# Kernel tuning notes

Hardware: AMD Instinct MI355X
Metric: run time of the kernel (lower is better)

Reference implementation:

```python
import jax, jax.numpy as jnp
import numpy as np

VOCAB, D, H1, H2, T = 32000, 256, 256, 256, 12
PAD, START, STOP = 0, 10, 11
B, S, NS = 32, 512, 16


def setup_inputs() -> dict:
    key = jax.random.key(0)
    ks = jax.random.split(key, 16)
    def rn(k, shape, scale=0.1):
        return (jax.random.normal(k, shape) * scale).astype(jnp.float32)
    inputs = jax.random.randint(ks[0], (B, S), 0, VOCAB)
    sent_embs = jax.random.normal(ks[1], (B, NS, 2 * H1), dtype=jnp.float32)
    embed = rn(ks[2], (VOCAB, D)).at[0].set(0.0)  # padding_idx=0
    # BiLSTM 1: input D, hidden H1; gate order i,f,g,o; dim 0 = [fwd, bwd]
    lstm1_wih = rn(ks[3], (2, 4 * H1, D))
    lstm1_whh = rn(ks[4], (2, 4 * H1, H1))
    lstm1_b = rn(ks[5], (2, 4 * H1))  # b_ih + b_hh fused
    # BiLSTM 2: input 4*H1 (= 2*2*lstm1_units), hidden H2
    lstm2_wih = rn(ks[6], (2, 4 * H2, 4 * H1))
    lstm2_whh = rn(ks[7], (2, 4 * H2, H2))
    lstm2_b = rn(ks[8], (2, 4 * H2))
    attW = rn(ks[9], (2 * H1, 2 * H1))
    h2t_w = rn(ks[10], (T, 2 * H2))
    h2t_b = rn(ks[11], (T,))
    trans = jax.random.normal(ks[12], (T, T), dtype=jnp.float32)
    trans = trans.at[START, :].set(-10000.0).at[:, STOP].set(-10000.0)
    return dict(inputs=inputs, sent_embs=sent_embs, embed=embed,
                lstm1_wih=lstm1_wih, lstm1_whh=lstm1_whh, lstm1_b=lstm1_b,
                lstm2_wih=lstm2_wih, lstm2_whh=lstm2_whh, lstm2_b=lstm2_b,
                attW=attW, h2t_w=h2t_w, h2t_b=h2t_b, trans=trans)


def _lstm_dir(x, wih, whh, b, reverse=False):
    # x: (S, B, Din) -> (S, B, H)
    if reverse:
        x = x[::-1]
    Hh = whh.shape[1]
    Bn = x.shape[1]
    def step(carry, xt):
        h, c = carry
        gates = xt @ wih.T + h @ whh.T + b
        i, f, g, o = jnp.split(gates, 4, axis=-1)
        c = jax.nn.sigmoid(f) * c + jax.nn.sigmoid(i) * jnp.tanh(g)
        h = jax.nn.sigmoid(o) * jnp.tanh(c)
        return (h, c), h
    init = (jnp.zeros((Bn, Hh), x.dtype), jnp.zeros((Bn, Hh), x.dtype))
    _, hs = jax.lax.scan(step, init, x)
    return hs[::-1] if reverse else hs


def _bilstm(x, wih, whh, b):
    fwd = _lstm_dir(x, wih[0], whh[0], b[0])
    bwd = _lstm_dir(x, wih[1], whh[1], b[1], reverse=True)
    return jnp.concatenate([fwd, bwd], axis=-1)


def _lstm_features(inputs, sent_embs, embed, lstm1_wih, lstm1_whh, lstm1_b,
                   lstm2_wih, lstm2_whh, lstm2_b, attW, h2t_w, h2t_b):
    emb = embed[inputs].transpose(1, 0, 2)            # (S,B,D); dropout is identity at eval
    l1 = _bilstm(emb, lstm1_wih, lstm1_whh, lstm1_b)  # (S,B,2H1)
    word = l1.transpose(1, 0, 2)                      # (B,S,2H1)
    wx = jnp.einsum('bse,fe->bsf', word, attW)        # Linear W (no bias)
    scores = jnp.einsum('bsf,bnf->bsn', wx, sent_embs)
    aw = jax.nn.softmax(scores, axis=-1)
    g = jnp.einsum('bsn,bnf->bsf', aw, sent_embs)
    comb = jnp.concatenate([wx, g], axis=-1)          # (B,S,4H1)
    l2 = _bilstm(comb.transpose(1, 0, 2), lstm2_wih, lstm2_whh, lstm2_b)  # (S,B,2H2)
    feats = jnp.einsum('sbf,tf->bst', l2, h2t_w) + h2t_b  # (B,S,T)
    return feats


def _viterbi(feats_b, trans):
    # feats_b: (S,T) -> (path (S,), score)
    init = jnp.full((T,), -10000.0, feats_b.dtype).at[START].set(0.0)
    def step(fv, feat):
        sc = fv[None, :] + trans          # [next, prev]
        bp = jnp.argmax(sc, axis=1)
        return jnp.max(sc, axis=1) + feat, bp
    fv, bps = jax.lax.scan(step, init, feats_b)
    term = fv + trans[STOP]
    best = jnp.argmax(term)
    def back(tag, bp):
        return bp[tag], tag
    _, path = jax.lax.scan(back, best, bps, reverse=True)
    return path, term[best]


def reference(inputs, sent_embs, embed, lstm1_wih, lstm1_whh, lstm1_b,
              lstm2_wih, lstm2_whh, lstm2_b, attW, h2t_w, h2t_b, trans):
    feats = _lstm_features(inputs, sent_embs, embed, lstm1_wih, lstm1_whh, lstm1_b,
                           lstm2_wih, lstm2_whh, lstm2_b, attW, h2t_w, h2t_b)
    paths, _ = jax.vmap(_viterbi, in_axes=(0, None))(feats, trans)
    return paths  # (B,S) predicted tag sequence
```

## Files before the change

kernel.cpp:

```cpp
#include <hip/hip_runtime.h>
#include <hip/hip_bf16.h>

#define BB 32
#define SS 512
#define DD 256
#define HH 256
#define GG 1024
#define MM (SS*BB)
#define NSENT 16
#define TT 12
#define TAG_START 10
#define TAG_STOP 11

typedef unsigned long long u64;
typedef unsigned int u32;

__device__ __forceinline__ float sigm(float x) {
  x = fminf(fmaxf(x, -15.f), 15.f);
  return 1.f / (1.f + __expf(-x));
}
__device__ __forceinline__ float tanh_fast(float x) {
  x = fminf(fmaxf(x, -15.f), 15.f);
  float e = __expf(2.f * x);
  return (e - 1.f) / (e + 1.f);
}

__global__ void embed_kernel(const int* __restrict__ toks, const float* __restrict__ emb,
                             float* __restrict__ X1) {
  int m = blockIdx.x;
  int s = m >> 5, b = m & 31;
  int tok = toks[b * SS + s];
  ((float4*)(X1 + (size_t)m * DD))[threadIdx.x] =
      ((const float4*)(emb + (size_t)tok * DD))[threadIdx.x];
}

__launch_bounds__(256)
__global__ void gemm_nt(const float* __restrict__ A, const float* __restrict__ W_,
                        const float* __restrict__ bias_, float* __restrict__ C_,
                        int K, int lda, int ldw, int ldC, size_t wz, size_t cz) {
  __shared__ float As[16 * 132];
  __shared__ float Ws[16 * 132];
  const float* W = W_ + (size_t)blockIdx.z * wz;
  const float* bias = bias_ ? bias_ + (size_t)blockIdx.z * GG : nullptr;
  float* C = C_ + (size_t)blockIdx.z * cz;
  const int tid = threadIdx.x;
  const int n0 = blockIdx.x * 128, m0 = blockIdx.y * 128;
  const int row = tid & 127, half = tid >> 7;
  const int tx = tid & 15, ty = tid >> 4;
  float acc[8][8] = {};
  const float* Arow = A + (size_t)(m0 + row) * lda;
  const float* Wrow = W + (size_t)(n0 + row) * ldw;
  for (int kk = 0; kk < K; kk += 16) {
    const int kb = half * 8;
    float4 a0 = *(const float4*)(Arow + kk + kb);
    float4 a1 = *(const float4*)(Arow + kk + kb + 4);
    float4 w0 = *(const float4*)(Wrow + kk + kb);
    float4 w1 = *(const float4*)(Wrow + kk + kb + 4);
    As[(kb + 0) * 132 + row] = a0.x; As[(kb + 1) * 132 + row] = a0.y;
    As[(kb + 2) * 132 + row] = a0.z; As[(kb + 3) * 132 + row] = a0.w;
    As[(kb + 4) * 132 + row] = a1.x; As[(kb + 5) * 132 + row] = a1.y;
    As[(kb + 6) * 132 + row] = a1.z; As[(kb + 7) * 132 + row] = a1.w;
    Ws[(kb + 0) * 132 + row] = w0.x; Ws[(kb + 1) * 132 + row] = w0.y;
    Ws[(kb + 2) * 132 + row] = w0.z; Ws[(kb + 3) * 132 + row] = w0.w;
    Ws[(kb + 4) * 132 + row] = w1.x; Ws[(kb + 5) * 132 + row] = w1.y;
    Ws[(kb + 6) * 132 + row] = w1.z; Ws[(kb + 7) * 132 + row] = w1.w;
    __syncthreads();
#pragma unroll
    for (int kl = 0; kl < 16; ++kl) {
      const float4 alo = *(const float4*)&As[kl * 132 + ty * 4];
      const float4 ahi = *(const float4*)&As[kl * 132 + 64 + ty * 4];
      const float4 wlo = *(const float4*)&Ws[kl * 132 + tx * 4];
      const float4 whi = *(const float4*)&Ws[kl * 132 + 64 + tx * 4];
      const float am[8] = {alo.x, alo.y, alo.z, alo.w, ahi.x, ahi.y, ahi.z, ahi.w};
      const float wm[8] = {wlo.x, wlo.y, wlo.z, wlo.w, whi.x, whi.y, whi.z, whi.w};
#pragma unroll
      for (int i = 0; i < 8; ++i)
#pragma unroll
        for (int j = 0; j < 8; ++j) acc[i][j] = fmaf(am[i], wm[j], acc[i][j]);
    }
    __syncthreads();
  }
  float4 blo = make_float4(0.f, 0.f, 0.f, 0.f), bhi = blo;
  if (bias) {
    blo = *(const float4*)(bias + n0 + tx * 4);
    bhi = *(const float4*)(bias + n0 + 64 + tx * 4);
  }
#pragma unroll
  for (int i = 0; i < 8; ++i) {
    const int m = m0 + ((i < 4) ? (ty * 4 + i) : (64 + ty * 4 + i - 4));
    float4 lo = make_float4(acc[i][0] + blo.x, acc[i][1] + blo.y,
                            acc[i][2] + blo.z, acc[i][3] + blo.w);
    float4 hi = make_float4(acc[i][4] + bhi.x, acc[i][5] + bhi.y,
                            acc[i][6] + bhi.z, acc[i][7] + bhi.w);
    *(float4*)(C + (size_t)m * ldC + n0 + tx * 4) = lo;
    *(float4*)(C + (size_t)m * ldC + n0 + 64 + tx * 4) = hi;
  }
}

__global__ void prep_whh(const float* __restrict__ whh1, const float* __restrict__ whh2,
                         float* __restrict__ o1, float* __restrict__ o2) {
  int idx0 = blockIdx.x * 256 + threadIdx.x;
  int layer = idx0 >> 19;
  int idx = idx0 & 524287;
  const float* whh = layer ? whh2 : whh1;
  float* out = layer ? o2 : o1;
  int c    = idx & 3;
  int t    = (idx >> 2) & 255;
  int i4   = (idx >> 10) & 31;
  int sl   = (idx >> 15) & 7;
  int d    = idx >> 18;
  int r    = t & 127;
  int half = t >> 7;
  int g = (r >> 5) * 256 + sl * 32 + (r & 31);
  int k = half * 128 + i4 * 4 + c;
  out[idx] = whh[(size_t)(d * GG + g) * HH + k];
}

__global__ void attadd_kernel(const float* __restrict__ aw, const float* __restrict__ sentW,
                              float* __restrict__ Xp) {
  __shared__ float a[NSENT];
  const int idx = blockIdx.x;
  const int d = idx >> 14;
  const int m = idx & (MM - 1);
  const int b = m & 31;
  const int tid = threadIdx.x;
  if (tid < NSENT) a[tid] = aw[(size_t)m * 16 + tid];
  __syncthreads();
  const int g = tid * 4;
  float* xp = Xp + ((size_t)d * MM + m) * GG + g;
  const float* swp = sentW + ((size_t)d * 512 + b * 16) * 1024 + g;
  float4 acc = *(const float4*)xp;
#pragma unroll
  for (int n = 0; n < NSENT; ++n) {
    const float4 sw = *(const float4*)&swp[(size_t)n * 1024];
    acc.x = fmaf(a[n], sw.x, acc.x);
    acc.y = fmaf(a[n], sw.y, acc.y);
    acc.z = fmaf(a[n], sw.z, acc.z);
    acc.w = fmaf(a[n], sw.w, acc.w);
  }
  *(float4*)xp = acc;
}

__launch_bounds__(256, 1)
__global__ void rec_kernel(const float* __restrict__ Xp, const float* __restrict__ whh_p,
                           float* __restrict__ hist, u64* __restrict__ hx) {
  __shared__ float h_lds[512];
  __shared__ float p_lds[512];
  const int tid = threadIdx.x;
  const int bid = blockIdx.x;
  const int sl = bid >> 5;
  const int db = bid & 31;
  const int d = db & 1;
  const int bg = db >> 1;
  const int r = tid & 127;
  const int half = tid >> 7;
  const float* wp = whh_p + (size_t)(d * 8 + sl) * 32768;
  float w[128];
#pragma unroll
  for (int i4 = 0; i4 < 32; ++i4) {
    const float4 v = *(const float4*)&wp[(size_t)(i4 * 256 + tid) * 4];
    w[i4 * 4 + 0] = v.x; w[i4 * 4 + 1] = v.y;
    w[i4 * 4 + 2] = v.z; w[i4 * 4 + 3] = v.w;
  }
  const float* XpD = Xp + (size_t)d * MM * GG;
  const int gcol = (r >> 5) * 256 + sl * 32 + (r & 31);
  const int jj = tid & 31, cc = tid >> 5;
  const int histMine = ((r >> 4) == sl);
  float creg = 0.f;
  u64* grp[2] = { hx + ((size_t)(0 * 2 + d) * 16 + bg) * 512,
                  hx + ((size_t)(1 * 2 + d) * 16 + bg) * 512 };
  float xn0 = 0.f, xn1 = 0.f;
  if (half == 0) {
    const int s0 = d ? (SS - 1) : 0;
    const int m00 = s0 * BB + bg * 2;
    xn0 = XpD[(size_t)m00 * GG + gcol];
    xn1 = XpD[(size_t)(m00 + 1) * GG + gcol];
  }
#pragma unroll 1
  for (int t = 0; t < SS; ++t) {
    const float x0 = xn0, x1 = xn1;
    u64 w0, w1;
    {
      u64* base = grp[t & 1] + tid * 2;
      w0 = __hip_atomic_load(base + 0, __ATOMIC_RELAXED, __HIP_MEMORY_SCOPE_AGENT);
      w1 = __hip_atomic_load(base + 1, __ATOMIC_RELAXED, __HIP_MEMORY_SCOPE_AGENT);
      while (((u32)(w0 >> 32) != (u32)t) | ((u32)(w1 >> 32) != (u32)t)) {
        __builtin_amdgcn_s_sleep(1);
        w0 = __hip_atomic_load(base + 0, __ATOMIC_RELAXED, __HIP_MEMORY_SCOPE_AGENT);
        w1 = __hip_atomic_load(base + 1, __ATOMIC_RELAXED, __HIP_MEMORY_SCOPE_AGENT);
      }
    }
    *(float2*)&h_lds[tid * 2] = make_float2(__uint_as_float((u32)w0),
                                            __uint_as_float((u32)w1));
    __syncthreads();
    {
      const int kb = half * 128;
      float p0a = 0.f, p0b = 0.f, p1a = 0.f, p1b = 0.f;
#pragma unroll
      for (int k8 = 0; k8 < 16; ++k8) {
        const float4 h0a = *(const float4*)&h_lds[kb + k8 * 8];
        const float4 h0b = *(const float4*)&h_lds[kb + k8 * 8 + 4];
        const float4 h1a = *(const float4*)&h_lds[256 + kb + k8 * 8];
        const float4 h1b = *(const float4*)&h_lds[256 + kb + k8 * 8 + 4];
        p0a = fmaf(w[k8*8+0], h0a.x, p0a); p0a = fmaf(w[k8*8+1], h0a.y, p0a);
        p0a = fmaf(w[k8*8+2], h0a.z, p0a); p0a = fmaf(w[k8*8+3], h0a.w, p0a);
        p0b = fmaf(w[k8*8+4], h0b.x, p0b); p0b = fmaf(w[k8*8+5], h0b.y, p0b);
        p0b = fmaf(w[k8*8+6], h0b.z, p0b); p0b = fmaf(w[k8*8+7], h0b.w, p0b);
        p1a = fmaf(w[k8*8+0], h1a.x, p1a); p1a = fmaf(w[k8*8+1], h1a.y, p1a);
        p1a = fmaf(w[k8*8+2], h1a.z, p1a); p1a = fmaf(w[k8*8+3], h1a.w, p1a);
        p1b = fmaf(w[k8*8+4], h1b.x, p1b); p1b = fmaf(w[k8*8+5], h1b.y, p1b);
        p1b = fmaf(w[k8*8+6], h1b.z, p1b); p1b = fmaf(w[k8*8+7], h1b.w, p1b);
      }
      *(float2*)&p_lds[tid * 2] = make_float2(p0a + p0b + x0, p1a + p1b + x1);
    }
    __syncthreads();
    if (tid < 64) {
      const float iv = p_lds[(jj) * 2 + cc]       + p_lds[(128 + jj) * 2 + cc];
      const float fv = p_lds[(32 + jj) * 2 + cc]  + p_lds[(128 + 32 + jj) * 2 + cc];
      const float gv = p_lds[(64 + jj) * 2 + cc]  + p_lds[(128 + 64 + jj) * 2 + cc];
      const float ov = p_lds[(96 + jj) * 2 + cc]  + p_lds[(128 + 96 + jj) * 2 + cc];
      const float cs = sigm(fv) * creg + sigm(iv) * tanh_fast(gv);
      creg = cs;
      const float hn = sigm(ov) * tanh_fast(cs);
      u64 wv = ((u64)(u32)(t + 1) << 32) | (u64)__float_as_uint(hn);
      __hip_atomic_store(grp[(t + 1) & 1] + cc * 256 + sl * 32 + jj, wv,
                         __ATOMIC_RELAXED, __HIP_MEMORY_SCOPE_AGENT);
    }
    if (histMine && t > 0) {
      const int sp = d ? (SS - t) : (t - 1);
      *(float2*)&hist[(size_t)(sp * BB + bg * 2 + half) * 512 + d * 256 + r * 2] =
          make_float2(__uint_as_float((u32)w0), __uint_as_float((u32)w1));
    }
    if (half == 0) {
      const int tn = (t + 1 < SS) ? (t + 1) : (SS - 1);
      const int sn = d ? (SS - 1 - tn) : tn;
      const int m0n = sn * BB + bg * 2;
      xn0 = XpD[(size_t)m0n * GG + gcol];
      xn1 = XpD[(size_t)(m0n + 1) * GG + gcol];
    }
  }
  if (histMine) {
    u64* base = grp[SS & 1] + tid * 2;
    u64 w0, w1;
    do {
      w0 = __hip_atomic_load(base + 0, __ATOMIC_RELAXED, __HIP_MEMORY_SCOPE_AGENT);
      w1 = __hip_atomic_load(base + 1, __ATOMIC_RELAXED, __HIP_MEMORY_SCOPE_AGENT);
      if (((u32)(w0 >> 32) == (u32)SS) & ((u32)(w1 >> 32) == (u32)SS)) break;
      __builtin_amdgcn_s_sleep(1);
    } while (true);
    const int sp = d ? 0 : (SS - 1);
    *(float2*)&hist[(size_t)(sp * BB + bg * 2 + half) * 512 + d * 256 + r * 2] =
        make_float2(__uint_as_float((u32)w0), __uint_as_float((u32)w1));
  }
}

__global__ void aw_kernel(const float* __restrict__ wx, const float* __restrict__ sent,
                          float* __restrict__ awout) {
  __shared__ float sl[NSENT * 512];
  __shared__ float wxr[512];
  __shared__ float parts[256];
  __shared__ float avals[NSENT];
  __shared__ float red0;
  const int tid = threadIdx.x;
  const int b = blockIdx.y;
  const int s0 = blockIdx.x * 32;
  for (int i = tid; i < NSENT * 512; i += 256) sl[i] = sent[(size_t)b * NSENT * 512 + i];
  __syncthreads();
  for (int si = 0; si < 32; ++si) {
    const int m = (s0 + si) * BB + b;
    for (int i = tid; i < 512; i += 256) wxr[i] = wx[(size_t)m * 512 + i];
    __syncthreads();
    const int n = tid >> 4, kp = tid & 15;
    float p = 0.f;
#pragma unroll 8
    for (int f = kp * 32; f < kp * 32 + 32; ++f) p = fmaf(wxr[f], sl[n * 512 + f], p);
    parts[tid] = p;
    __syncthreads();
    if (tid < NSENT) {
      float sc = 0.f;
      for (int qq = 0; qq < 16; ++qq) sc += parts[tid * 16 + qq];
      avals[tid] = sc;
    }
    __syncthreads();
    if (tid == 0) {
      float mx = avals[0];
      for (int qq = 1; qq < NSENT; ++qq) mx = fmaxf(mx, avals[qq]);
      float sm = 0.f;
      for (int qq = 0; qq < NSENT; ++qq) { float e = expf(avals[qq] - mx); avals[qq] = e; sm += e; }
      red0 = 1.f / sm;
    }
    __syncthreads();
    if (tid < NSENT) awout[(size_t)m * 16 + tid] = avals[tid] * red0;
    __syncthreads();
  }
}

__global__ void feats_kernel(const float* __restrict__ l2m, const float* __restrict__ w,
                             const float* __restrict__ bias, float* __restrict__ feats) {
  const int wave = threadIdx.x >> 6, lane = threadIdx.x & 63;
  const int m = blockIdx.x * 4 + wave;
  const float* row = l2m + (size_t)m * 512;
  float rv[8];
#pragma unroll
  for (int i = 0; i < 8; ++i) rv[i] = row[lane + i * 64];
  for (int t = 0; t < TT; ++t) {
    const float* wr = w + t * 512;
    float p = 0.f;
#pragma unroll
    for (int i = 0; i < 8; ++i) p = fmaf(rv[i], wr[lane + i * 64], p);
#pragma unroll
    for (int off = 32; off; off >>= 1) p += __shfl_down(p, off);
    if (lane == 0) feats[(size_t)m * TT + t] = p + bias[t];
  }
}

__global__ void viterbi_kernel(const float* __restrict__ feats, const float* __restrict__ trans,
                               int* __restrict__ out) {
  __shared__ float flds[SS * TT];
  __shared__ unsigned char bp[SS * TT];
  __shared__ float tr[TT * TT];
  __shared__ float fv[TT];
  __shared__ float tv[TT];
  __shared__ int pathS[SS];
  const int b = blockIdx.x, tid = threadIdx.x;
  for (int i = tid; i < SS * TT; i += 64) {
    int s = i / TT, t = i - s * TT;
    flds[i] = feats[(size_t)(s * BB + b) * TT + t];
  }
  for (int i = tid; i < TT * TT; i += 64) tr[i] = trans[i];
  if (tid < TT) fv[tid] = (tid == TAG_START) ? 0.f : -10000.f;
  __syncthreads();
  for (int s = 0; s < SS; ++s) {
    float nf = 0.f;
    if (tid < TT) {
      float mx = -1e30f;
      int bj = 0;
#pragma unroll
      for (int jj = 0; jj < TT; ++jj) {
        float v = fv[jj] + tr[tid * TT + jj];
        if (v > mx) { mx = v; bj = jj; }
      }
      nf = mx + flds[s * TT + tid];
      bp[s * TT + tid] = (unsigned char)bj;
    }
    __syncthreads();
    if (tid < TT) fv[tid] = nf;
    __syncthreads();
  }
  if (tid < TT) tv[tid] = fv[tid] + tr[TAG_STOP * TT + tid];
  __syncthreads();
  if (tid == 0) {
    int best = 0;
    float mx = tv[0];
    for (int jj = 1; jj < TT; ++jj)
      if (tv[jj] > mx) { mx = tv[jj]; best = jj; }
    pathS[SS - 1] = best;
    for (int s = SS - 1; s > 0; --s) { best = bp[s * TT + best]; pathS[s - 1] = best; }
  }
  __syncthreads();
  for (int s = tid; s < SS; s += 64) out[b * SS + s] = pathS[s];
}

#define OFF_XP    ((size_t)0)
#define OFF_WX    ((size_t)134217728)
#define OFF_L2M   ((size_t)167772160)
#define OFF_WORD  ((size_t)201326592)
#define OFF_WT1   ((size_t)234881024)
#define OFF_WT2   ((size_t)236978176)
#define OFF_FEATS ((size_t)239075328)
#define OFF_HX1   ((size_t)239861760)
#define OFF_HX2   ((size_t)240123904)
#define OFF_SENTW ((size_t)240386048)
#define OFF_AW    ((size_t)244580352)

extern "C" void kernel_launch(void* const* d_in, const int* in_sizes, int n_in,
                              void* d_out, int out_size, void* d_ws, size_t ws_size,
                              hipStream_t stream) {
  const int* inputs  = (const int*)d_in[0];
  const float* sent  = (const float*)d_in[1];
  const float* emb   = (const float*)d_in[2];
  const float* l1wih = (const float*)d_in[3];
  const float* l1whh = (const float*)d_in[4];
  const float* l1b   = (const float*)d_in[5];
  const float* l2wih = (const float*)d_in[6];
  const float* l2whh = (const float*)d_in[7];
  const float* l2b   = (const float*)d_in[8];
  const float* attW  = (const float*)d_in[9];
  const float* h2tw  = (const float*)d_in[10];
  const float* h2tb  = (const float*)d_in[11];
  const float* trans = (const float*)d_in[12];
  int* out = (int*)d_out;
  char* ws = (char*)d_ws;

  float* Xp    = (float*)(ws + OFF_XP);
  float* wx    = (float*)(ws + OFF_WX);
  float* l2m   = (float*)(ws + OFF_L2M);
  float* X1    = l2m;
  float* word  = (float*)(ws + OFF_WORD);
  float* wt1   = (float*)(ws + OFF_WT1);
  float* wt2   = (float*)(ws + OFF_WT2);
  float* feats = (float*)(ws + OFF_FEATS);
  u64* hx1     = (u64*)(ws + OFF_HX1);
  u64* hx2     = (u64*)(ws + OFF_HX2);
  float* sentW = (float*)(ws + OFF_SENTW);
  float* awb   = (float*)(ws + OFF_AW);

  (void)hipMemsetAsync(ws + OFF_HX1, 0, 262144 * 2, stream);

  prep_whh<<<4096, 256, 0, stream>>>(l1whh, l2whh, wt1, wt2);
  gemm_nt<<<dim3(8, 4, 2), 256, 0, stream>>>(sent, l2wih + 512, nullptr, sentW,
                                             512, 512, GG, 1024,
                                             (size_t)GG * GG, (size_t)512 * 1024);
  embed_kernel<<<MM, 64, 0, stream>>>(inputs, emb, X1);
  gemm_nt<<<dim3(8, 128, 2), 256, 0, stream>>>(X1, l1wih, l1b, Xp,
                                               DD, DD, DD, GG,
                                               (size_t)GG * DD, (size_t)MM * GG);
  rec_kernel<<<256, 256, 0, stream>>>(Xp, wt1, word, hx1);
  gemm_nt<<<dim3(4, 128, 1), 256, 0, stream>>>(word, attW, nullptr, wx,
                                               512, 512, 512, 512, 0, 0);
  aw_kernel<<<dim3(16, 32), 256, 0, stream>>>(wx, sent, awb);
  gemm_nt<<<dim3(8, 128, 2), 256, 0, stream>>>(wx, l2wih, l2b, Xp,
                                               512, 512, GG, GG,
                                               (size_t)GG * GG, (size_t)MM * GG);
  attadd_kernel<<<2 * MM, 256, 0, stream>>>(awb, sentW, Xp);
  rec_kernel<<<256, 256, 0, stream>>>(Xp, wt2, l2m, hx2);
  feats_kernel<<<MM / 4, 256, 0, stream>>>(l2m, h2tw, h2tb, feats);
  viterbi_kernel<<<BB, 64, 0, stream>>>(feats, trans, out);
}
```

Baseline: 3.910 ms.

## Repartition LSTM recurrence over 4 slices of 512 threads instead of 8

The persistent recurrent kernel now splits the gate rows into 4 slices per direction/batch-pair with 512-thread blocks (128 blocks) instead of 8 slices with 256 threads (256 blocks). Each block owns 64 hidden units, so fewer blocks participate in the per-step global flag exchange and each thread polls one flag word instead of two. The weight prepack permutation is updated to match. The trade-off is fewer active CUs and a larger per-block barrier with 512 threads, each still holding 128 weight registers.

```diff
diff --git a/kernel.cpp b/kernel.cpp
--- a/kernel.cpp
+++ b/kernel.cpp
@@ -105,13 +105,13 @@
   const float* whh = layer ? whh2 : whh1;
   float* out = layer ? o2 : o1;
   int c    = idx & 3;
-  int t    = (idx >> 2) & 255;
-  int i4   = (idx >> 10) & 31;
-  int sl   = (idx >> 15) & 7;
+  int t    = (idx >> 2) & 511;
+  int i4   = (idx >> 11) & 31;
+  int sl2  = (idx >> 16) & 3;
   int d    = idx >> 18;
-  int r    = t & 127;
-  int half = t >> 7;
-  int g = (r >> 5) * 256 + sl * 32 + (r & 31);
+  int r2   = t & 255;
+  int half = t >> 8;
+  int g = (r2 >> 6) * 256 + sl2 * 64 + (r2 & 63);
   int k = half * 128 + i4 * 4 + c;
   out[idx] = whh[(size_t)(d * GG + g) * HH + k];
 }
@@ -141,31 +141,31 @@
   *(float4*)xp = acc;
 }
 
-__launch_bounds__(256, 1)
+__launch_bounds__(512, 1)
 __global__ void rec_kernel(const float* __restrict__ Xp, const float* __restrict__ whh_p,
                            float* __restrict__ hist, u64* __restrict__ hx) {
   __shared__ float h_lds[512];
-  __shared__ float p_lds[512];
+  __shared__ float p_lds[1024];
   const int tid = threadIdx.x;
   const int bid = blockIdx.x;
-  const int sl = bid >> 5;
+  const int sl2 = bid >> 5;
   const int db = bid & 31;
   const int d = db & 1;
   const int bg = db >> 1;
-  const int r = tid & 127;
-  const int half = tid >> 7;
-  const float* wp = whh_p + (size_t)(d * 8 + sl) * 32768;
+  const int r2 = tid & 255;
+  const int half = tid >> 8;
+  const float* wp = whh_p + (size_t)(d * 4 + sl2) * 65536;
   float w[128];
 #pragma unroll
   for (int i4 = 0; i4 < 32; ++i4) {
-    const float4 v = *(const float4*)&wp[(size_t)(i4 * 256 + tid) * 4];
+    const float4 v = *(const float4*)&wp[(size_t)(i4 * 512 + tid) * 4];
     w[i4 * 4 + 0] = v.x; w[i4 * 4 + 1] = v.y;
     w[i4 * 4 + 2] = v.z; w[i4 * 4 + 3] = v.w;
   }
   const float* XpD = Xp + (size_t)d * MM * GG;
-  const int gcol = (r >> 5) * 256 + sl * 32 + (r & 31);
-  const int jj = tid & 31, cc = tid >> 5;
-  const int histMine = ((r >> 4) == sl);
+  const int gcol = (r2 >> 6) * 256 + sl2 * 64 + (r2 & 63);
+  const int jj = tid & 63, cc = tid >> 6;
+  const int histMine = (((tid & 255) >> 6) == sl2);
   float creg = 0.f;
   u64* grp[2] = { hx + ((size_t)(0 * 2 + d) * 16 + bg) * 512,
                   hx + ((size_t)(1 * 2 + d) * 16 + bg) * 512 };
@@ -179,19 +179,16 @@
 #pragma unroll 1
   for (int t = 0; t < SS; ++t) {
     const float x0 = xn0, x1 = xn1;
-    u64 w0, w1;
+    u64 w0;
     {
-      u64* base = grp[t & 1] + tid * 2;
-      w0 = __hip_atomic_load(base + 0, __ATOMIC_RELAXED, __HIP_MEMORY_SCOPE_AGENT);
-      w1 = __hip_atomic_load(base + 1, __ATOMIC_RELAXED, __HIP_MEMORY_SCOPE_AGENT);
-      while (((u32)(w0 >> 32) != (u32)t) | ((u32)(w1 >> 32) != (u32)t)) {
+      u64* base = grp[t & 1] + tid;
+      w0 = __hip_atomic_load(base, __ATOMIC_RELAXED, __HIP_MEMORY_SCOPE_AGENT);
+      while ((u32)(w0 >> 32) != (u32)t) {
         __builtin_amdgcn_s_sleep(1);
-        w0 = __hip_atomic_load(base + 0, __ATOMIC_RELAXED, __HIP_MEMORY_SCOPE_AGENT);
-        w1 = __hip_atomic_load(base + 1, __ATOMIC_RELAXED, __HIP_MEMORY_SCOPE_AGENT);
+        w0 = __hip_atomic_load(base, __ATOMIC_RELAXED, __HIP_MEMORY_SCOPE_AGENT);
       }
     }
-    *(float2*)&h_lds[tid * 2] = make_float2(__uint_as_float((u32)w0),
-                                            __uint_as_float((u32)w1));
+    h_lds[tid] = __uint_as_float((u32)w0);
     __syncthreads();
     {
       const int kb = half * 128;
@@ -214,22 +211,22 @@
       *(float2*)&p_lds[tid * 2] = make_float2(p0a + p0b + x0, p1a + p1b + x1);
     }
     __syncthreads();
-    if (tid < 64) {
-      const float iv = p_lds[(jj) * 2 + cc]       + p_lds[(128 + jj) * 2 + cc];
-      const float fv = p_lds[(32 + jj) * 2 + cc]  + p_lds[(128 + 32 + jj) * 2 + cc];
-      const float gv = p_lds[(64 + jj) * 2 + cc]  + p_lds[(128 + 64 + jj) * 2 + cc];
-      const float ov = p_lds[(96 + jj) * 2 + cc]  + p_lds[(128 + 96 + jj) * 2 + cc];
+    if (tid < 128) {
+      const float iv = p_lds[(jj) * 2 + cc]        + p_lds[(256 + jj) * 2 + cc];
+      const float fv = p_lds[(64 + jj) * 2 + cc]   + p_lds[(256 + 64 + jj) * 2 + cc];
+      const float gv = p_lds[(128 + jj) * 2 + cc]  + p_lds[(256 + 128 + jj) * 2 + cc];
+      const float ov = p_lds[(192 + jj) * 2 + cc]  + p_lds[(256 + 192 + jj) * 2 + cc];
       const float cs = sigm(fv) * creg + sigm(iv) * tanh_fast(gv);
       creg = cs;
       const float hn = sigm(ov) * tanh_fast(cs);
       u64 wv = ((u64)(u32)(t + 1) << 32) | (u64)__float_as_uint(hn);
-      __hip_atomic_store(grp[(t + 1) & 1] + cc * 256 + sl * 32 + jj, wv,
+      __hip_atomic_store(grp[(t + 1) & 1] + cc * 256 + sl2 * 64 + jj, wv,
                          __ATOMIC_RELAXED, __HIP_MEMORY_SCOPE_AGENT);
     }
     if (histMine && t > 0) {
       const int sp = d ? (SS - t) : (t - 1);
-      *(float2*)&hist[(size_t)(sp * BB + bg * 2 + half) * 512 + d * 256 + r * 2] =
-          make_float2(__uint_as_float((u32)w0), __uint_as_float((u32)w1));
+      hist[(size_t)(sp * BB + bg * 2 + (tid >> 8)) * 512 + d * 256 + (tid & 255)] =
+          __uint_as_float((u32)w0);
     }
     if (half == 0) {
       const int tn = (t + 1 < SS) ? (t + 1) : (SS - 1);
@@ -240,17 +237,16 @@
     }
   }
   if (histMine) {
-    u64* base = grp[SS & 1] + tid * 2;
-    u64 w0, w1;
+    u64* base = grp[SS & 1] + tid;
+    u64 w0;
     do {
-      w0 = __hip_atomic_load(base + 0, __ATOMIC_RELAXED, __HIP_MEMORY_SCOPE_AGENT);
-      w1 = __hip_atomic_load(base + 1, __ATOMIC_RELAXED, __HIP_MEMORY_SCOPE_AGENT);
-      if (((u32)(w0 >> 32) == (u32)SS) & ((u32)(w1 >> 32) == (u32)SS)) break;
+      w0 = __hip_atomic_load(base, __ATOMIC_RELAXED, __HIP_MEMORY_SCOPE_AGENT);
+      if ((u32)(w0 >> 32) == (u32)SS) break;
       __builtin_amdgcn_s_sleep(1);
     } while (true);
     const int sp = d ? 0 : (SS - 1);
-    *(float2*)&hist[(size_t)(sp * BB + bg * 2 + half) * 512 + d * 256 + r * 2] =
-        make_float2(__uint_as_float((u32)w0), __uint_as_float((u32)w1));
+    hist[(size_t)(sp * BB + bg * 2 + (tid >> 8)) * 512 + d * 256 + (tid & 255)] =
+        __uint_as_float((u32)w0);
   }
 }
 
@@ -415,7 +411,7 @@
   gemm_nt<<<dim3(8, 128, 2), 256, 0, stream>>>(X1, l1wih, l1b, Xp,
                                                DD, DD, DD, GG,
                                                (size_t)GG * DD, (size_t)MM * GG);
-  rec_kernel<<<256, 256, 0, stream>>>(Xp, wt1, word, hx1);
+  rec_kernel<<<128, 512, 0, stream>>>(Xp, wt1, word, hx1);
   gemm_nt<<<dim3(4, 128, 1), 256, 0, stream>>>(word, attW, nullptr, wx,
                                                512, 512, 512, 512, 0, 0);
   aw_kernel<<<dim3(16, 32), 256, 0, stream>>>(wx, sent, awb);
@@ -423,7 +419,7 @@
                                                512, 512, GG, GG,
                                                (size_t)GG * GG, (size_t)MM * GG);
   attadd_kernel<<<2 * MM, 256, 0, stream>>>(awb, sentW, Xp);
-  rec_kernel<<<256, 256, 0, stream>>>(Xp, wt2, l2m, hx2);
+  rec_kernel<<<128, 512, 0, stream>>>(Xp, wt2, l2m, hx2);
   feats_kernel<<<MM / 4, 256, 0, stream>>>(l2m, h2tw, h2tb, feats);
   viterbi_kernel<<<BB, 64, 0, stream>>>(feats, trans, out);
 }
```

Result: slower. 6.253 ms (+59.9%).

## Split layer-1 LSTM recurrence across 4 slices with 512-thread blocks

Applied to the files above, without the earlier changes.

Adds a new recurrent kernel for layer 1 that uses 128 blocks of 512 threads, each owning 64 hidden units per gate (4 slices instead of 8), and a matching weight-permutation path in prep_whh. Fewer blocks take part in the per-timestep cross-block handshake through global atomics, which is meant to reduce synchronisation latency on the sequential critical path. The cost is more work per block per step, the same 128 weights per thread in registers, and an extra LDS reduction over two halves of K. Layer 2 still uses the old kernel.

```diff
diff --git a/kernel.cpp b/kernel.cpp
--- a/kernel.cpp
+++ b/kernel.cpp
@@ -102,18 +102,29 @@
   int idx0 = blockIdx.x * 256 + threadIdx.x;
   int layer = idx0 >> 19;
   int idx = idx0 & 524287;
-  const float* whh = layer ? whh2 : whh1;
-  float* out = layer ? o2 : o1;
-  int c    = idx & 3;
-  int t    = (idx >> 2) & 255;
-  int i4   = (idx >> 10) & 31;
-  int sl   = (idx >> 15) & 7;
-  int d    = idx >> 18;
-  int r    = t & 127;
-  int half = t >> 7;
-  int g = (r >> 5) * 256 + sl * 32 + (r & 31);
-  int k = half * 128 + i4 * 4 + c;
-  out[idx] = whh[(size_t)(d * GG + g) * HH + k];
+  if (layer == 0) {
+    int c    = idx & 3;
+    int t    = (idx >> 2) & 511;
+    int i4   = (idx >> 11) & 31;
+    int sl2  = (idx >> 16) & 3;
+    int d    = idx >> 18;
+    int r2   = t & 255;
+    int half = t >> 8;
+    int g = (r2 >> 6) * 256 + sl2 * 64 + (r2 & 63);
+    int k = half * 128 + i4 * 4 + c;
+    o1[idx] = whh1[(size_t)(d * GG + g) * HH + k];
+  } else {
+    int c    = idx & 3;
+    int t    = (idx >> 2) & 255;
+    int i4   = (idx >> 10) & 31;
+    int sl   = (idx >> 15) & 7;
+    int d    = idx >> 18;
+    int r    = t & 127;
+    int half = t >> 7;
+    int g = (r >> 5) * 256 + sl * 32 + (r & 31);
+    int k = half * 128 + i4 * 4 + c;
+    o2[idx] = whh2[(size_t)(d * GG + g) * HH + k];
+  }
 }
 
 __global__ void attadd_kernel(const float* __restrict__ aw, const float* __restrict__ sentW,
@@ -139,6 +150,115 @@
     acc.w = fmaf(a[n], sw.w, acc.w);
   }
   *(float4*)xp = acc;
+}
+
+__attribute__((amdgpu_flat_work_group_size(512, 512), amdgpu_waves_per_eu(2, 2)))
+__global__ void rec_kernel_v2(const float* __restrict__ Xp, const float* __restrict__ whh_p,
+                              float* __restrict__ hist, u64* __restrict__ hx) {
+  __shared__ float h_lds[512];
+  __shared__ float p_lds[1024];
+  const int tid = threadIdx.x;
+  const int bid = blockIdx.x;
+  const int sl2 = bid >> 5;
+  const int db = bid & 31;
+  const int d = db & 1;
+  const int bg = db >> 1;
+  const int r2 = tid & 255;
+  const int half = tid >> 8;
+  const float* wp = whh_p + (size_t)(d * 4 + sl2) * 65536;
+  float w[128];
+#pragma unroll
+  for (int i4 = 0; i4 < 32; ++i4) {
+    const float4 v = *(const float4*)&wp[(size_t)(i4 * 512 + tid) * 4];
+    w[i4 * 4 + 0] = v.x; w[i4 * 4 + 1] = v.y;
+    w[i4 * 4 + 2] = v.z; w[i4 * 4 + 3] = v.w;
+  }
+  const float* XpD = Xp + (size_t)d * MM * GG;
+  const int gcol = (r2 >> 6) * 256 + sl2 * 64 + (r2 & 63);
+  const int jj = tid & 63, cc = tid >> 6;
+  const int histMine = (((tid & 255) >> 6) == sl2);
+  float creg = 0.f;
+  u64* grp[2] = { hx + ((size_t)(0 * 2 + d) * 16 + bg) * 512,
+                  hx + ((size_t)(1 * 2 + d) * 16 + bg) * 512 };
+  float xn0 = 0.f, xn1 = 0.f;
+  if (half == 0) {
+    const int s0 = d ? (SS - 1) : 0;
+    const int m00 = s0 * BB + bg * 2;
+    xn0 = XpD[(size_t)m00 * GG + gcol];
+    xn1 = XpD[(size_t)(m00 + 1) * GG + gcol];
+  }
+#pragma unroll 1
+  for (int t = 0; t < SS; ++t) {
+    const float x0 = xn0, x1 = xn1;
+    u64 w0;
+    {
+      u64* base = grp[t & 1] + tid;
+      w0 = __hip_atomic_load(base, __ATOMIC_RELAXED, __HIP_MEMORY_SCOPE_AGENT);
+      while ((u32)(w0 >> 32) != (u32)t) {
+        __builtin_amdgcn_s_sleep(1);
+        w0 = __hip_atomic_load(base, __ATOMIC_RELAXED, __HIP_MEMORY_SCOPE_AGENT);
+      }
+    }
+    h_lds[tid] = __uint_as_float((u32)w0);
+    __syncthreads();
+    {
+      const int kb = half * 128;
+      float p0a = 0.f, p0b = 0.f, p1a = 0.f, p1b = 0.f;
+#pragma unroll
+      for (int k8 = 0; k8 < 16; ++k8) {
+        const float4 h0a = *(const float4*)&h_lds[kb + k8 * 8];
+        const float4 h0b = *(const float4*)&h_lds[kb + k8 * 8 + 4];
+        const float4 h1a = *(const float4*)&h_lds[256 + kb + k8 * 8];
+        const float4 h1b = *(const float4*)&h_lds[256 + kb + k8 * 8 + 4];
+        p0a = fmaf(w[k8*8+0], h0a.x, p0a); p0a = fmaf(w[k8*8+1], h0a.y, p0a);
+        p0a = fmaf(w[k8*8+2], h0a.z, p0a); p0a = fmaf(w[k8*8+3], h0a.w, p0a);
+        p0b = fmaf(w[k8*8+4], h0b.x, p0b); p0b = fmaf(w[k8*8+5], h0b.y, p0b);
+        p0b = fmaf(w[k8*8+6], h0b.z, p0b); p0b = fmaf(w[k8*8+7], h0b.w, p0b);
+        p1a = fmaf(w[k8*8+0], h1a.x, p1a); p1a = fmaf(w[k8*8+1], h1a.y, p1a);
+        p1a = fmaf(w[k8*8+2], h1a.z, p1a); p1a = fmaf(w[k8*8+3], h1a.w, p1a);
+        p1b = fmaf(w[k8*8+4], h1b.x, p1b); p1b = fmaf(w[k8*8+5], h1b.y, p1b);
+        p1b = fmaf(w[k8*8+6], h1b.z, p1b); p1b = fmaf(w[k8*8+7], h1b.w, p1b);
+      }
+      *(float2*)&p_lds[tid * 2] = make_float2(p0a + p0b + x0, p1a + p1b + x1);
+    }
+    __syncthreads();
+    if (tid < 128) {
+      const float iv = p_lds[(jj) * 2 + cc]        + p_lds[(256 + jj) * 2 + cc];
+      const float fv = p_lds[(64 + jj) * 2 + cc]   + p_lds[(256 + 64 + jj) * 2 + cc];
+      const float gv = p_lds[(128 + jj) * 2 + cc]  + p_lds[(256 + 128 + jj) * 2 + cc];
+      const float ov = p_lds[(192 + jj) * 2 + cc]  + p_lds[(256 + 192 + jj) * 2 + cc];
+      const float cs = sigm(fv) * creg + sigm(iv) * tanh_fast(gv);
+      creg = cs;
+      const float hn = sigm(ov) * tanh_fast(cs);
+      u64 wv = ((u64)(u32)(t + 1) << 32) | (u64)__float_as_uint(hn);
+      __hip_atomic_store(grp[(t + 1) & 1] + cc * 256 + sl2 * 64 + jj, wv,
+                         __ATOMIC_RELAXED, __HIP_MEMORY_SCOPE_AGENT);
+    }
+    if (histMine && t > 0) {
+      const int sp = d ? (SS - t) : (t - 1);
+      hist[(size_t)(sp * BB + bg * 2 + (tid >> 8)) * 512 + d * 256 + (tid & 255)] =
+          __uint_as_float((u32)w0);
+    }
+    if (half == 0) {
+      const int tn = (t + 1 < SS) ? (t + 1) : (SS - 1);
+      const int sn = d ? (SS - 1 - tn) : tn;
+      const int m0n = sn * BB + bg * 2;
+      xn0 = XpD[(size_t)m0n * GG + gcol];
+      xn1 = XpD[(size_t)(m0n + 1) * GG + gcol];
+    }
+  }
+  if (histMine) {
+    u64* base = grp[SS & 1] + tid;
+    u64 w0;
+    do {
+      w0 = __hip_atomic_load(base, __ATOMIC_RELAXED, __HIP_MEMORY_SCOPE_AGENT);
+      if ((u32)(w0 >> 32) == (u32)SS) break;
+      __builtin_amdgcn_s_sleep(1);
+    } while (true);
+    const int sp = d ? 0 : (SS - 1);
+    hist[(size_t)(sp * BB + bg * 2 + (tid >> 8)) * 512 + d * 256 + (tid & 255)] =
+        __uint_as_float((u32)w0);
+  }
 }
 
 __launch_bounds__(256, 1)
@@ -415,7 +535,7 @@
   gemm_nt<<<dim3(8, 128, 2), 256, 0, stream>>>(X1, l1wih, l1b, Xp,
                                                DD, DD, DD, GG,
                                                (size_t)GG * DD, (size_t)MM * GG);
-  rec_kernel<<<256, 256, 0, stream>>>(Xp, wt1, word, hx1);
+  rec_kernel_v2<<<128, 512, 0, stream>>>(Xp, wt1, word, hx1);
   gemm_nt<<<dim3(4, 128, 1), 256, 0, stream>>>(word, attW, nullptr, wx,
                                                512, 512, 512, 512, 0, 0);
   aw_kernel<<<dim3(16, 32), 256, 0, stream>>>(wx, sent, awb);
```

After: 5.215 ms. 33.4% more time.
